# Performance work log

Measured on AMD Instinct MI355X. Metric: run time of the kernel, lower is better.

The kernel has to match this reference:

```python
import jax, jax.numpy as jnp
import numpy as np

V, E, H, M = 256, 512, 512, 128
D = 2 * H  # decoder hidden
B, L_TXT, T_MEL = 32, 256, 800
EPS = 1e-5


def setup_inputs() -> dict:
    key = jax.random.key(0)
    ks = jax.random.split(key, 24)
    s = 0.02
    inp = {
        'x': jax.random.randint(ks[0], (B, L_TXT), 0, V),
        'text_seq_lens': jax.random.randint(ks[1], (B,), 1, L_TXT + 1),
        'y': jax.random.normal(ks[2], (B, T_MEL, M), jnp.float32),
        'mel_spec_lens': jax.random.randint(ks[3], (B,), 1, T_MEL + 1),
        'emb': jax.random.normal(ks[4], (V, E)) * s,
        'conv1_w': jax.random.normal(ks[5], (E, E, 3)) * s,
        'conv1_b': jnp.zeros((E,)),
        'bn1_g': jnp.ones((E,)), 'bn1_b': jnp.zeros((E,)),
        'conv2_w': jax.random.normal(ks[6], (E, E, 3)) * s,
        'conv2_b': jnp.zeros((E,)),
        'bn2_g': jnp.ones((E,)), 'bn2_b': jnp.zeros((E,)),
        'wih_f': jax.random.normal(ks[7], (4 * H, E)) * s,
        'whh_f': jax.random.normal(ks[8], (4 * H, H)) * s,
        'bih_f': jnp.zeros((4 * H,)), 'bhh_f': jnp.zeros((4 * H,)),
        'wih_b': jax.random.normal(ks[9], (4 * H, E)) * s,
        'whh_b': jax.random.normal(ks[10], (4 * H, H)) * s,
        'bih_b': jnp.zeros((4 * H,)), 'bhh_b': jnp.zeros((4 * H,)),
        'dwih': jax.random.normal(ks[11], (4 * D, M)) * s,
        'dwhh': jax.random.normal(ks[12], (4 * D, D)) * s,
        'dbih': jnp.zeros((4 * D,)), 'dbhh': jnp.zeros((4 * D,)),
        'proj_w': jax.random.normal(ks[13], (M, D)) * s,
        'proj_b': jnp.zeros((M,)),
        'gate_w': jax.random.normal(ks[14], (1, D)) * s,
        'gate_b': jnp.zeros((1,)),
    }
    return inp


def _conv_bn_relu(x, w, b, g, beta):
    # x: (B, E, L); training-mode BatchNorm (batch statistics, biased var)
    x = jax.lax.conv_general_dilated(x, w, (1,), [(1, 1)],
                                     dimension_numbers=('NCH', 'OIH', 'NCH')) + b[None, :, None]
    mu = jnp.mean(x, axis=(0, 2), keepdims=True)
    var = jnp.mean((x - mu) ** 2, axis=(0, 2), keepdims=True)
    x = (x - mu) * jax.lax.rsqrt(var + EPS) * g[None, :, None] + beta[None, :, None]
    return jax.nn.relu(x)


def _lstm_last(xseq, lens, wih, whh, bih, bhh):
    # Run LSTM over full padded seq, freezing state past each length.
    # Returns final (h, c) == state at t = len-1 (packed-sequence semantics).
    Bb, T, _ = xseq.shape
    Hh = whh.shape[1]
    pre = jnp.einsum('bte,ge->btg', xseq, wih) + bih + bhh  # (B,T,4H)

    def step(carry, inp):
        h, c = carry
        xt, t = inp
        gates = xt + h @ whh.T
        i, f, g, o = jnp.split(gates, 4, axis=-1)
        c_n = jax.nn.sigmoid(f) * c + jax.nn.sigmoid(i) * jnp.tanh(g)
        h_n = jax.nn.sigmoid(o) * jnp.tanh(c_n)
        valid = (t < lens)[:, None]
        return (jnp.where(valid, h_n, h), jnp.where(valid, c_n, c)), None

    init = (jnp.zeros((Bb, Hh), xseq.dtype), jnp.zeros((Bb, Hh), xseq.dtype))
    (h, c), _ = jax.lax.scan(step, init, (pre.transpose(1, 0, 2), jnp.arange(T)))
    return h, c


def _forward(x, text_seq_lens, y, mel_spec_lens, emb, conv1_w, conv1_b, bn1_g, bn1_b,
             conv2_w, conv2_b, bn2_g, bn2_b, wih_f, whh_f, bih_f, bhh_f,
             wih_b, whh_b, bih_b, bhh_b, dwih, dwhh, dbih, dbhh,
             proj_w, proj_b, gate_w, gate_b):
    xe = emb[x]                       # (B, L, E)
    h = xe.transpose(0, 2, 1)         # (B, E, L)
    h = _conv_bn_relu(h, conv1_w, conv1_b, bn1_g, bn1_b)  # dropout = identity (eval)
    h = _conv_bn_relu(h, conv2_w, conv2_b, bn2_g, bn2_b)
    h = h.transpose(0, 2, 1)          # (B, L, E)

    # bidirectional encoder LSTM final states (packed semantics)
    hf, cf = _lstm_last(h, text_seq_lens, wih_f, whh_f, bih_f, bhh_f)
    # reverse each sequence within its valid length for the backward direction
    t_idx = jnp.arange(h.shape[1])[None, :]
    rev_idx = jnp.clip(text_seq_lens[:, None] - 1 - t_idx, 0, h.shape[1] - 1)
    h_rev = jnp.take_along_axis(h, rev_idx[:, :, None], axis=1)
    hb, cb = _lstm_last(h_rev, text_seq_lens, wih_b, whh_b, bih_b, bhh_b)

    hid = jnp.concatenate([hf, hb], axis=1)  # (B, 2H)
    cel = jnp.concatenate([cf, cb], axis=1)

    Tm = y.shape[1]

    def dec_step(carry, _):
        hd, cd, inp = carry
        gates = inp @ dwih.T + dbih + dbhh + hd @ dwhh.T
        i, f, g, o = jnp.split(gates, 4, axis=-1)
        cd = jax.nn.sigmoid(f) * cd + jax.nn.sigmoid(i) * jnp.tanh(g)
        hd = jax.nn.sigmoid(o) * jnp.tanh(cd)
        mel = hd @ proj_w.T + proj_b          # (B, M)
        gate = hd @ gate_w.T + gate_b         # (B, 1)
        return (hd, cd, mel), (mel, gate[:, 0])

    sos = jnp.zeros((y.shape[0], M), y.dtype)
    _, (mels, gates) = jax.lax.scan(dec_step, (hid, cel, sos), None, length=Tm)
    mel_outputs = mels.transpose(1, 0, 2)     # (B, Tm, M)
    gate_outputs = gates.T                    # (B, Tm)

    mask = jnp.arange(Tm)[None, :] > mel_spec_lens[:, None]  # (B, Tm), strictly >
    masked_mel = jnp.where(mask[:, :, None], 0.0, mel_outputs)
    masked_gate = jnp.where(mask, 1000.0, gate_outputs)
    return masked_mel, masked_gate, mask


def reference(x, text_seq_lens, y, mel_spec_lens, emb, conv1_w, conv1_b, bn1_g, bn1_b,
              conv2_w, conv2_b, bn2_g, bn2_b, wih_f, whh_f, bih_f, bhh_f,
              wih_b, whh_b, bih_b, bhh_b, dwih, dwhh, dbih, dbhh,
              proj_w, proj_b, gate_w, gate_b):
    return _forward(x, text_seq_lens, y, mel_spec_lens, emb, conv1_w, conv1_b,
                    bn1_g, bn1_b, conv2_w, conv2_b, bn2_g, bn2_b,
                    wih_f, whh_f, bih_f, bhh_f, wih_b, whh_b, bih_b, bhh_b,
                    dwih, dwhh, dbih, dbhh, proj_w, proj_b, gate_w, gate_b)
```

## Files before the change

kernel.cpp:

```cpp
#include <hip/hip_runtime.h>


typedef float f4 __attribute__((ext_vector_type(4)));
typedef _Float16 h8 __attribute__((ext_vector_type(8)));
typedef _Float16 half_t;
typedef unsigned long long u64;

#define B_    32
#define LTXT  256
#define TMEL  800
#define EE    512
#define HH    512
#define DD    1024
#define MM    128
#define NROWS 8192
#define GATE_OFF 3276800
#define MASK_OFF 3302400

#define RING_D 801
#define RING_E 257
#define HOP    13

#define WS_MBE        0ull
#define WS_MBD        16384ull
#define WS_HENC       49152ull
#define WS_ZERO_BYTES 81920ull
#define WS_HD         16891904ull
#define WS_BUFX       69386240ull
#define WS_BUFY       77774848ull
#define WS_CONVF      86163456ull
#define WS_WEFF       86163456ull
#define WS_W0         94552064ull
#define WS_WP1        102940672ull
#define WS_WP2        104513536ull
#define WS_WIHP       106086400ull
#define WS_WHHP       110280704ull
#define WS_BSUM       114475008ull
#define WS_BEFF       114491392ull
#define WS_B0         114507776ull
#define WS_MEAN       114524160ull
#define WS_RSTD       114526208ull
#define WS_PROJW      114528256ull
#define WS_PROJG      114790400ull
#define WS_CEL        114823168ull

__device__ __forceinline__ float sigm(float x) { return 1.f / (1.f + __expf(-x)); }
__device__ __forceinline__ float tanh_f(float x) {
    float e = __expf(2.f * x);
    return 1.f - 2.f / (e + 1.f);
}

__device__ __forceinline__ void st_atom64(void* p, u64 v) {
    asm volatile("global_atomic_swap_x2 %0, %1, off" :: "v"(p), "v"(v) : "memory");
}
__device__ __forceinline__ void st_atom32(unsigned* p, unsigned v) {
    asm volatile("global_atomic_swap %0, %1, off" :: "v"(p), "v"(v) : "memory");
}


__global__ void k_embed(const int* __restrict__ x, const float* __restrict__ emb,
                        half_t* __restrict__ out) {
    int row = blockIdx.x;
    int tok = x[row];
    const float* e = emb + (size_t)tok * EE;
    half_t* o = out + (size_t)row * EE;
    for (int c = threadIdx.x; c < EE; c += blockDim.x) o[c] = (half_t)e[c];
}

__global__ void k_packconvw(const float* __restrict__ w, half_t* __restrict__ wp) {
    int idx = blockIdx.x * 256 + threadIdx.x;
    if (idx >= 3 * EE * EE) return;
    int s = idx / (EE * EE);
    int rem = idx - s * EE * EE;
    int eo = rem >> 9, ei = rem & 511;
    wp[idx] = (half_t)w[(size_t)eo * (EE * 3) + ei * 3 + s];
}

__global__ __launch_bounds__(256) void k_conv(const half_t* __restrict__ A,
                                              const half_t* __restrict__ Wp,
                                              const float* __restrict__ bias,
                                              float* __restrict__ out) {
    const int nt = blockIdx.x, et = blockIdx.y;
    const int tid = threadIdx.x;
    const int wv = tid >> 6, l = tid & 63, quad = l >> 4, lo = l & 15;
    const int rowA = nt * 64 + wv * 16 + lo;
    const int eo = et * 16 + lo;
    f4 acc = {0.f, 0.f, 0.f, 0.f};
    for (int s = 0; s < 3; ++s) {
        int lsp = (rowA & 255) + s - 1;
        bool valid = (lsp >= 0) && (lsp < 256);
        int rs = rowA + s - 1;
        rs = rs < 0 ? 0 : (rs > NROWS - 1 ? NROWS - 1 : rs);
        const half_t* ab = A + (size_t)rs * EE;
        const half_t* wb = Wp + ((size_t)s * EE + eo) * EE;
#pragma unroll 4
        for (int ks = 0; ks < 16; ++ks) {
            h8 a = {0, 0, 0, 0, 0, 0, 0, 0};
            if (valid) a = *(const h8*)(ab + ks * 32 + quad * 8);
            h8 b = *(const h8*)(wb + ks * 32 + quad * 8);
            acc = __builtin_amdgcn_mfma_f32_16x16x32_f16(a, b, acc, 0, 0, 0);
        }
    }
    const int orow = nt * 64 + wv * 16 + quad * 4;
    const float bv = bias[eo];
#pragma unroll
    for (int r = 0; r < 4; ++r) out[(size_t)(orow + r) * EE + eo] = acc[r] + bv;
}

__global__ __launch_bounds__(256) void k_bnstats(const float* __restrict__ x,
                                                 float* __restrict__ mean,
                                                 float* __restrict__ rstd) {
    const int c = blockIdx.x;
    float s = 0.f, ss = 0.f;
    for (int n = threadIdx.x; n < NROWS; n += 256) {
        float v = x[(size_t)n * EE + c];
        s += v; ss += v * v;
    }
#pragma unroll
    for (int off = 32; off > 0; off >>= 1) { s += __shfl_down(s, off); ss += __shfl_down(ss, off); }
    __shared__ float as[4], ass[4];
    int wv = threadIdx.x >> 6;
    if ((threadIdx.x & 63) == 0) { as[wv] = s; ass[wv] = ss; }
    __syncthreads();
    if (threadIdx.x == 0) {
        float S = as[0] + as[1] + as[2] + as[3];
        float SS = ass[0] + ass[1] + ass[2] + ass[3];
        float m = S / (float)NROWS;
        float var = SS / (float)NROWS - m * m;
        mean[c] = m;
        rstd[c] = rsqrtf(var + 1e-5f);
    }
}

__global__ void k_bnapply(const float* __restrict__ x, const float* __restrict__ mean,
                          const float* __restrict__ rstd, const float* __restrict__ g,
                          const float* __restrict__ beta, half_t* __restrict__ out) {
    int idx = blockIdx.x * 256 + threadIdx.x;
    if (idx >= NROWS * EE) return;
    int c = idx & (EE - 1);
    float v = (x[idx] - mean[c]) * rstd[c] * g[c] + beta[c];
    out[idx] = (half_t)(v > 0.f ? v : 0.f);
}

__global__ void k_packrec(const float* __restrict__ src, half_t* __restrict__ dst,
                          int Hdim, int kshift, int total) {
    int idx = blockIdx.x * 256 + threadIdx.x;
    if (idx >= total) return;
    int p = idx >> kshift;
    int k = idx & ((1 << kshift) - 1);
    int he = p >> 2, g = p & 3;
    dst[idx] = (half_t)src[((size_t)g * Hdim + he) * (size_t)(1 << kshift) + k];
}

__global__ void k_bsumenc(const float* __restrict__ bf, const float* __restrict__ bhf,
                          const float* __restrict__ bb, const float* __restrict__ bhb,
                          float* __restrict__ bsum) {
    int p = blockIdx.x * 256 + threadIdx.x;
    if (p >= 4096) return;
    int dir = p >> 11, pp = p & 2047;
    int he = pp >> 2, g = pp & 3;
    int row = g * HH + he;
    bsum[p] = dir ? (bb[row] + bhb[row]) : (bf[row] + bhf[row]);
}

__global__ __launch_bounds__(256) void k_weff(const float* __restrict__ dwhh,
                                              const float* __restrict__ dwih,
                                              const float* __restrict__ projw,
                                              half_t* __restrict__ weff,
                                              half_t* __restrict__ w0) {
    int row = blockIdx.x;
    int k = blockIdx.y * 256 + threadIdx.x;
    float v = dwhh[(size_t)row * DD + k];
    float acc = v;
    for (int m = 0; m < MM; ++m) acc += dwih[(size_t)row * MM + m] * projw[(size_t)m * DD + k];
    int p = ((row & (DD - 1)) << 2) | (row >> 10);
    weff[(size_t)p * DD + k] = (half_t)acc;
    w0[(size_t)p * DD + k] = (half_t)v;
}

__global__ void k_bdec(const float* __restrict__ dbih, const float* __restrict__ dbhh,
                       const float* __restrict__ dwih, const float* __restrict__ projb,
                       float* __restrict__ beff, float* __restrict__ b0) {
    int p = blockIdx.x * 256 + threadIdx.x;
    if (p >= 4096) return;
    int he = p >> 2, g = p & 3;
    int row = g * DD + he;
    float bb = dbih[row] + dbhh[row];
    float acc = bb;
    for (int m = 0; m < MM; ++m) acc += dwih[(size_t)row * MM + m] * projb[m];
    b0[p] = bb;
    beff[p] = acc;
}

__global__ void k_cast(const float* __restrict__ src, half_t* __restrict__ dst, int n) {
    int idx = blockIdx.x * 256 + threadIdx.x;
    if (idx < n) dst[idx] = (half_t)src[idx];
}

__global__ void k_projg(const float* __restrict__ gw, half_t* __restrict__ pg) {
    int idx = blockIdx.x * 256 + threadIdx.x;
    if (idx >= 16 * DD) return;
    int row = idx >> 10, k = idx & (DD - 1);
    pg[idx] = (half_t)(row == 0 ? gw[k] : 0.f);
}

__global__ void k_mask(const int* __restrict__ lens, float* __restrict__ out) {
    int idx = blockIdx.x * 256 + threadIdx.x;
    if (idx >= B_ * TMEL) return;
    int b = idx / TMEL, t = idx - b * TMEL;
    out[MASK_OFF + idx] = (t > lens[b]) ? 1.f : 0.f;
}

__global__ __launch_bounds__(512) void k_enc(const half_t* __restrict__ X,
                                             const half_t* __restrict__ wihp,
                                             const half_t* __restrict__ whhp,
                                             const float* __restrict__ bsum,
                                             const int* __restrict__ lens,
                                             half_t* __restrict__ henc,
                                             half_t* __restrict__ hd0,
                                             float* __restrict__ cel,
                                             unsigned* __restrict__ mbE) {
    const int j = blockIdx.x;
    const int dir = j >> 5, sub = j & 31;
    const int tid = threadIdx.x;
    const int wv = tid >> 6, l = tid & 63, quad = l >> 4, lo = l & 15;
    const int rg = wv >> 1, bh = wv & 1;
    const int bfr = bh * 16 + lo;
    const int ue = tid >> 5, ub = tid & 31;

    __shared__ half_t s_hd[32 * 520];
    __shared__ float s_g[32][65];
    __shared__ float s_c[16][32];
    __shared__ float s_h[16][32];
    __shared__ half_t s_hh[16][32];
    __shared__ int s_len[32];

    if (tid < 32) s_len[tid] = lens[tid];
    s_c[ue][ub] = 0.f;
    s_h[ue][ub] = 0.f;

    const int pr = dir * 2048 + sub * 64 + rg * 16 + lo;
    const half_t* wih_b = wihp + (size_t)pr * 512;
    const half_t* whh_b = whhp + (size_t)pr * 512;
    const float bias_n = bsum[pr];

    h8 wihreg[16], whhreg[16];
#pragma unroll
    for (int ks = 0; ks < 16; ++ks) {
        wihreg[ks] = *(const h8*)(wih_b + ks * 32 + quad * 8);
        whhreg[ks] = *(const h8*)(whh_b + ks * 32 + quad * 8);
    }

    int sp = 0, sn = HOP;
    __syncthreads();

    for (int t = 0; t < 256; ++t) {
        if (t > 0) {
            if (tid >= 64 && tid < 96) {
                const unsigned want = (unsigned)t;
                const unsigned* fp = mbE + (size_t)(dir * 32 + sub) * 64 + (tid - 64);
                while (__hip_atomic_load(fp, __ATOMIC_RELAXED, __HIP_MEMORY_SCOPE_AGENT) < want)
                    __builtin_amdgcn_s_sleep(1);
            }
            __syncthreads();
        }

        const half_t* src = henc + (size_t)sp * 32768 + (size_t)dir * 16384;
        h8 tmp0 = *(const h8*)(src + (size_t)(tid + 0 * 512) * 8);
        h8 tmp1 = *(const h8*)(src + (size_t)(tid + 1 * 512) * 8);
        h8 tmp2 = *(const h8*)(src + (size_t)(tid + 2 * 512) * 8);
        h8 tmp3 = *(const h8*)(src + (size_t)(tid + 3 * 512) * 8);

        const int lb = s_len[bfr];
        int tt = (dir == 0) ? t : (lb - 1 - t);
        tt = tt < 0 ? 0 : tt;
        const half_t* xr = X + ((size_t)bfr * 256 + tt) * 512;
        f4 accA = {0.f, 0.f, 0.f, 0.f}, accB = {0.f, 0.f, 0.f, 0.f};
#pragma unroll
        for (int ks = 0; ks < 16; ++ks) {
            h8 a = *(const h8*)(xr + ks * 32 + quad * 8);
            accA = __builtin_amdgcn_mfma_f32_16x16x32_f16(a, wihreg[ks], accA, 0, 0, 0);
        }

        {
            int c0 = tid;
            *(h8*)(s_hd + (size_t)(c0 >> 6) * 520 + (c0 & 63) * 8) = tmp0;
            int c1 = tid + 512;
            *(h8*)(s_hd + (size_t)(c1 >> 6) * 520 + (c1 & 63) * 8) = tmp1;
            int c2 = tid + 1024;
            *(h8*)(s_hd + (size_t)(c2 >> 6) * 520 + (c2 & 63) * 8) = tmp2;
            int c3 = tid + 1536;
            *(h8*)(s_hd + (size_t)(c3 >> 6) * 520 + (c3 & 63) * 8) = tmp3;
        }
        __syncthreads();

#pragma unroll
        for (int ks = 0; ks < 16; ++ks) {
            h8 a = *(const h8*)(s_hd + (size_t)bfr * 520 + ks * 32 + quad * 8);
            accB = __builtin_amdgcn_mfma_f32_16x16x32_f16(a, whhreg[ks], accB, 0, 0, 0);
        }
        const int bm = bh * 16 + quad * 4, cm = rg * 16 + lo;
#pragma unroll
        for (int r = 0; r < 4; ++r) s_g[bm + r][cm] = accA[r] + accB[r] + bias_n;
        __syncthreads();
        {
            float gi = s_g[ub][ue * 4 + 0], gf = s_g[ub][ue * 4 + 1];
            float gg = s_g[ub][ue * 4 + 2], go = s_g[ub][ue * 4 + 3];
            float cn = sigm(gf) * s_c[ue][ub] + sigm(gi) * tanh_f(gg);
            float hn = sigm(go) * tanh_f(cn);
            if (t < s_len[ub]) { s_c[ue][ub] = cn; s_h[ue][ub] = hn; }
            s_hh[ue][ub] = (half_t)s_h[ue][ub];
        }
        __syncthreads();
        if (tid < 64 && t < 255) {
            int b2 = tid >> 1, e8 = (tid & 1) * 8;
            union { half_t h[8]; u64 u[2]; } pk;
#pragma unroll
            for (int i = 0; i < 8; ++i) pk.h[i] = s_hh[e8 + i][b2];
            half_t* dst = henc + (size_t)sn * 32768 + (size_t)dir * 16384
                          + (size_t)b2 * 512 + sub * 16 + e8;
            st_atom64(dst, pk.u[0]);
            st_atom64(dst + 4, pk.u[1]);
            asm volatile("s_waitcnt vmcnt(0)");
            if (tid < 32)
                st_atom32(mbE + ((size_t)(dir * 32 + tid) * 64 + sub), (unsigned)(t + 1));
        }
        if (t < 255) { sp = sn; sn += HOP; if (sn >= RING_E) sn -= RING_E; }
    }
    hd0[(size_t)ub * 1024 + dir * 512 + sub * 16 + ue] = (half_t)s_h[ue][ub];
    cel[(size_t)ub * 1024 + dir * 512 + sub * 16 + ue] = s_c[ue][ub];
}

__global__ __launch_bounds__(512) void k_dec(const half_t* __restrict__ Weff,
                                             const half_t* __restrict__ W0,
                                             const float* __restrict__ beff,
                                             const float* __restrict__ b0,
                                             const half_t* __restrict__ projwb,
                                             const half_t* __restrict__ projg,
                                             const float* __restrict__ projb,
                                             const float* __restrict__ gateb,
                                             const int* __restrict__ mlens,
                                             const float* __restrict__ cel,
                                             half_t* __restrict__ hd,
                                             float* __restrict__ out,
                                             unsigned* __restrict__ mbD) {
    const int j = blockIdx.x;
    const int tid = threadIdx.x;
    const int wv = tid >> 6, l = tid & 63, quad = l >> 4, lo = l & 15;

    __shared__ half_t s_hd[32 * 1032];
    __shared__ float s_g[32][65];
    __shared__ float s_c[16][32];
    __shared__ half_t s_hh[16][32];
    __shared__ int s_len[32];

    if (j < 64) {
        const int rg = wv >> 1, bh = wv & 1;
        const int bfr = bh * 16 + lo;
        const int ue = tid >> 5, ub = tid & 31;

        s_c[ue][ub] = cel[(size_t)ub * 1024 + j * 16 + ue];
        const int pr = j * 64 + rg * 16 + lo;
        const float biasE = beff[pr], bias0 = b0[pr];
        const half_t* wbE = Weff + (size_t)pr * 1024;
        const half_t* wb0 = W0 + (size_t)pr * 1024;

        h8 wreg[32];
#pragma unroll
        for (int ks = 0; ks < 32; ++ks)
            wreg[ks] = *(const h8*)(wbE + ks * 32 + quad * 8);

        int sp = 0, sn = HOP;
        __syncthreads();

        for (int t = 1; t <= TMEL; ++t) {
            if (t > 1) {
                if (tid >= 64 && tid < 128) {
                    const unsigned want = (unsigned)(t - 1);
                    const unsigned* fp = mbD + (size_t)j * 64 + (tid - 64);
                    while (__hip_atomic_load(fp, __ATOMIC_RELAXED, __HIP_MEMORY_SCOPE_AGENT) < want)
                        __builtin_amdgcn_s_sleep(1);
                }
                __syncthreads();
            }

            const half_t* src = hd + (size_t)sp * 32768;
            {
                h8 tp[8];
#pragma unroll
                for (int i = 0; i < 8; ++i)
                    tp[i] = *(const h8*)(src + (size_t)(tid + i * 512) * 8);
#pragma unroll
                for (int i = 0; i < 8; ++i) {
                    int c = tid + i * 512;
                    *(h8*)(s_hd + (size_t)(c >> 7) * 1032 + (c & 127) * 8) = tp[i];
                }
            }
            __syncthreads();

            const half_t* ar = s_hd + (size_t)bfr * 1032 + quad * 8;
            f4 acc = {0.f, 0.f, 0.f, 0.f}, acc2 = {0.f, 0.f, 0.f, 0.f};
            if (t == 1) {
#pragma unroll 8
                for (int ks = 0; ks < 32; ks += 2) {
                    h8 a0 = *(const h8*)(ar + ks * 32);
                    h8 a1 = *(const h8*)(ar + ks * 32 + 32);
                    acc = __builtin_amdgcn_mfma_f32_16x16x32_f16(a0, *(const h8*)(wb0 + ks * 32 + quad * 8), acc, 0, 0, 0);
                    acc2 = __builtin_amdgcn_mfma_f32_16x16x32_f16(a1, *(const h8*)(wb0 + ks * 32 + 32 + quad * 8), acc2, 0, 0, 0);
                }
            } else {
#pragma unroll
                for (int ks = 0; ks < 32; ks += 2) {
                    h8 a0 = *(const h8*)(ar + ks * 32);
                    h8 a1 = *(const h8*)(ar + ks * 32 + 32);
                    acc = __builtin_amdgcn_mfma_f32_16x16x32_f16(a0, wreg[ks], acc, 0, 0, 0);
                    acc2 = __builtin_amdgcn_mfma_f32_16x16x32_f16(a1, wreg[ks + 1], acc2, 0, 0, 0);
                }
            }
            const float bn = (t == 1) ? bias0 : biasE;
            const int bm = bh * 16 + quad * 4, cm = rg * 16 + lo;
#pragma unroll
            for (int r = 0; r < 4; ++r) s_g[bm + r][cm] = acc[r] + acc2[r] + bn;
            __syncthreads();
            {
                float gi = s_g[ub][ue * 4 + 0], gf = s_g[ub][ue * 4 + 1];
                float gg = s_g[ub][ue * 4 + 2], go = s_g[ub][ue * 4 + 3];
                float cn = sigm(gf) * s_c[ue][ub] + sigm(gi) * tanh_f(gg);
                s_c[ue][ub] = cn;
                s_hh[ue][ub] = (half_t)(sigm(go) * tanh_f(cn));
            }
            __syncthreads();
            if (tid < 64) {
                int b2 = tid >> 1, e8 = (tid & 1) * 8;
                union { half_t h[8]; u64 u[2]; } pk;
#pragma unroll
                for (int i = 0; i < 8; ++i) pk.h[i] = s_hh[e8 + i][b2];
                half_t* dst = hd + (size_t)sn * 32768 + (size_t)b2 * 1024 + j * 16 + e8;
                st_atom64(dst, pk.u[0]);
                st_atom64(dst + 4, pk.u[1]);
                asm volatile("s_waitcnt vmcnt(0)");
                st_atom32(mbD + ((size_t)tid * 64 + j), (unsigned)t);
                if (tid < 9)
                    st_atom32(mbD + ((size_t)(64 + tid) * 64 + j), (unsigned)t);
            }
            sp = sn; sn += HOP; if (sn >= RING_D) sn -= RING_D;
        }
    } else {
        const int pj = j - 64;
        const bool meld = (pj < 8);
        const bool duty = (wv < 2);
        const int bh2 = wv & 1;
        const half_t* pw = meld ? (projwb + (size_t)(pj * 16 + lo) * 1024)
                                : (projg + (size_t)lo * 1024);
        const float biasP = meld ? projb[pj * 16 + lo] : gateb[0];

        h8 pwreg[32];
        if (duty) {
#pragma unroll
            for (int ks = 0; ks < 32; ++ks)
                pwreg[ks] = *(const h8*)(pw + ks * 32 + quad * 8);
        }
        if (tid < 32) s_len[tid] = mlens[tid];

        int spP = HOP;
        __syncthreads();

        for (int t = 1; t <= TMEL; ++t) {
            if (tid < 64) {
                const unsigned want = (unsigned)t;
                const unsigned* fp = mbD + (size_t)(64 + pj) * 64 + tid;
                while (__hip_atomic_load(fp, __ATOMIC_RELAXED, __HIP_MEMORY_SCOPE_AGENT) < want)
                    __builtin_amdgcn_s_sleep(1);
            }
            __syncthreads();

            const half_t* src = hd + (size_t)spP * 32768;
            {
                h8 tp[8];
#pragma unroll
                for (int i = 0; i < 8; ++i)
                    tp[i] = *(const h8*)(src + (size_t)(tid + i * 512) * 8);
#pragma unroll
                for (int i = 0; i < 8; ++i) {
                    int c = tid + i * 512;
                    *(h8*)(s_hd + (size_t)(c >> 7) * 1032 + (c & 127) * 8) = tp[i];
                }
            }
            __syncthreads();

            if (duty) {
                const half_t* ar = s_hd + (size_t)(bh2 * 16 + lo) * 1032 + quad * 8;
                f4 accm = {0.f, 0.f, 0.f, 0.f}, accm2 = {0.f, 0.f, 0.f, 0.f};
#pragma unroll
                for (int ks = 0; ks < 32; ks += 2) {
                    h8 a0 = *(const h8*)(ar + ks * 32);
                    h8 a1 = *(const h8*)(ar + ks * 32 + 32);
                    accm = __builtin_amdgcn_mfma_f32_16x16x32_f16(a0, pwreg[ks], accm, 0, 0, 0);
                    accm2 = __builtin_amdgcn_mfma_f32_16x16x32_f16(a1, pwreg[ks + 1], accm2, 0, 0, 0);
                }
                accm[0] += accm2[0]; accm[1] += accm2[1];
                accm[2] += accm2[2]; accm[3] += accm2[3];
                const int pos = t - 1;
                if (meld) {
#pragma unroll
                    for (int r = 0; r < 4; ++r) {
                        int b = bh2 * 16 + quad * 4 + r;
                        float v = accm[r] + biasP;
                        if (pos > s_len[b]) v = 0.f;
                        __builtin_nontemporal_store(v,
                            &out[(size_t)b * (TMEL * MM) + (size_t)pos * MM + pj * 16 + lo]);
                    }
                } else if (lo == 0) {
#pragma unroll
                    for (int r = 0; r < 4; ++r) {
                        int b = bh2 * 16 + quad * 4 + r;
                        float v = accm[r] + biasP;
                        if (pos > s_len[b]) v = 1000.f;
                        __builtin_nontemporal_store(v, &out[GATE_OFF + (size_t)b * TMEL + pos]);
                    }
                }
            }
            __syncthreads();
            spP += HOP; if (spP >= RING_D) spP -= RING_D;
        }
    }
}


extern "C" void kernel_launch(void* const* d_in, const int* in_sizes, int n_in,
                              void* d_out, int out_size, void* d_ws, size_t ws_size,
                              hipStream_t stream) {
    const int* x = (const int*)d_in[0];
    const int* tlens = (const int*)d_in[1];
    const int* mlens = (const int*)d_in[3];
    const float* emb = (const float*)d_in[4];
    const float* c1w = (const float*)d_in[5];
    const float* c1b = (const float*)d_in[6];
    const float* bn1g = (const float*)d_in[7];
    const float* bn1b = (const float*)d_in[8];
    const float* c2w = (const float*)d_in[9];
    const float* c2b = (const float*)d_in[10];
    const float* bn2g = (const float*)d_in[11];
    const float* bn2b = (const float*)d_in[12];
    const float* wihf = (const float*)d_in[13];
    const float* whhf = (const float*)d_in[14];
    const float* bihf = (const float*)d_in[15];
    const float* bhhf = (const float*)d_in[16];
    const float* wihb = (const float*)d_in[17];
    const float* whhb = (const float*)d_in[18];
    const float* bihb = (const float*)d_in[19];
    const float* bhhb = (const float*)d_in[20];
    const float* dwih = (const float*)d_in[21];
    const float* dwhh = (const float*)d_in[22];
    const float* dbih = (const float*)d_in[23];
    const float* dbhh = (const float*)d_in[24];
    const float* projw = (const float*)d_in[25];
    const float* projb = (const float*)d_in[26];
    const float* gatew = (const float*)d_in[27];
    const float* gateb = (const float*)d_in[28];
    float* out = (float*)d_out;
    char* ws = (char*)d_ws;

    unsigned* mbE = (unsigned*)(ws + WS_MBE);
    unsigned* mbD = (unsigned*)(ws + WS_MBD);
    half_t* henc = (half_t*)(ws + WS_HENC);
    half_t* hd = (half_t*)(ws + WS_HD);
    half_t* bufX = (half_t*)(ws + WS_BUFX);
    half_t* bufY = (half_t*)(ws + WS_BUFY);
    float* convf = (float*)(ws + WS_CONVF);
    half_t* weff = (half_t*)(ws + WS_WEFF);
    half_t* w0 = (half_t*)(ws + WS_W0);
    half_t* wp1 = (half_t*)(ws + WS_WP1);
    half_t* wp2 = (half_t*)(ws + WS_WP2);
    float* meanb = (float*)(ws + WS_MEAN);
    float* rstdb = (float*)(ws + WS_RSTD);
    half_t* wihp = (half_t*)(ws + WS_WIHP);
    half_t* whhp = (half_t*)(ws + WS_WHHP);
    float* bsum = (float*)(ws + WS_BSUM);
    float* beff = (float*)(ws + WS_BEFF);
    float* b0 = (float*)(ws + WS_B0);
    half_t* projwb = (half_t*)(ws + WS_PROJW);
    half_t* projg = (half_t*)(ws + WS_PROJG);
    float* cel = (float*)(ws + WS_CEL);

    hipMemsetAsync(d_ws, 0, (size_t)WS_ZERO_BYTES, stream);

    k_embed<<<NROWS, 256, 0, stream>>>(x, emb, bufX);
    k_packconvw<<<(3 * EE * EE + 255) / 256, 256, 0, stream>>>(c1w, wp1);
    k_conv<<<dim3(128, 32), 256, 0, stream>>>(bufX, wp1, c1b, convf);
    k_bnstats<<<EE, 256, 0, stream>>>(convf, meanb, rstdb);
    k_bnapply<<<(NROWS * EE) / 256, 256, 0, stream>>>(convf, meanb, rstdb, bn1g, bn1b, bufY);
    k_packconvw<<<(3 * EE * EE + 255) / 256, 256, 0, stream>>>(c2w, wp2);
    k_conv<<<dim3(128, 32), 256, 0, stream>>>(bufY, wp2, c2b, convf);
    k_bnstats<<<EE, 256, 0, stream>>>(convf, meanb, rstdb);
    k_bnapply<<<(NROWS * EE) / 256, 256, 0, stream>>>(convf, meanb, rstdb, bn2g, bn2b, bufX);

    const int encTot = 2048 * 512;
    k_packrec<<<(encTot + 255) / 256, 256, 0, stream>>>(wihf, wihp, HH, 9, encTot);
    k_packrec<<<(encTot + 255) / 256, 256, 0, stream>>>(wihb, wihp + encTot, HH, 9, encTot);
    k_packrec<<<(encTot + 255) / 256, 256, 0, stream>>>(whhf, whhp, HH, 9, encTot);
    k_packrec<<<(encTot + 255) / 256, 256, 0, stream>>>(whhb, whhp + encTot, HH, 9, encTot);
    k_bsumenc<<<16, 256, 0, stream>>>(bihf, bhhf, bihb, bhhb, bsum);

    k_enc<<<64, 512, 0, stream>>>(bufX, wihp, whhp, bsum, tlens, henc, hd, cel, mbE);

    k_weff<<<dim3(4096, 4), 256, 0, stream>>>(dwhh, dwih, projw, weff, w0);
    k_bdec<<<16, 256, 0, stream>>>(dbih, dbhh, dwih, projb, beff, b0);
    k_cast<<<(MM * DD + 255) / 256, 256, 0, stream>>>(projw, projwb, MM * DD);
    k_projg<<<(16 * DD + 255) / 256, 256, 0, stream>>>(gatew, projg);

    k_dec<<<73, 512, 0, stream>>>(weff, w0, beff, b0, projwb, projg, projb, gateb,
                                  mlens, cel, hd, out, mbD);

    k_mask<<<(B_ * TMEL + 255) / 256, 256, 0, stream>>>(mlens, out);

    (void)in_sizes; (void)n_in; (void)out_size; (void)ws_size;
}
```

Measured before the change: 4.901 ms.

## Split decoder recurrence into two independent batch groups with separate rings and mailboxes

The persistent decoder kernel now splits the batch of 32 into two independent groups of 16. Each group has its own hidden-state ring, its own mailbox flags and 32 recurrent blocks, with each block covering 128 gate rows instead of 64. Each group's blocks only wait on the 32 blocks of their own group, so there are fewer flags to poll and less hidden state to copy into shared memory per step. The projection and gate blocks are reorganised into one pair per group. The trade-off is that each block now loads weights for twice as many rows, and the encoder's final hidden-state write and the zeroed workspace size change to match the new layout.

Measured after the change: 4.482 ms. 8.6% less time.

```diff
diff --git a/kernel.cpp b/kernel.cpp
--- a/kernel.cpp
+++ b/kernel.cpp
@@ -24,7 +24,7 @@
 #define WS_MBE        0ull
 #define WS_MBD        16384ull
 #define WS_HENC       49152ull
-#define WS_ZERO_BYTES 81920ull
+#define WS_ZERO_BYTES 114688ull
 #define WS_HD         16891904ull
 #define WS_BUFX       69386240ull
 #define WS_BUFY       77774848ull
@@ -217,7 +217,7 @@
                                              const float* __restrict__ bsum,
                                              const int* __restrict__ lens,
                                              half_t* __restrict__ henc,
-                                             half_t* __restrict__ hd0,
+                                             half_t* __restrict__ hd,
                                              float* __restrict__ cel,
                                              unsigned* __restrict__ mbE) {
     const int j = blockIdx.x;
@@ -327,7 +327,11 @@
         }
         if (t < 255) { sp = sn; sn += HOP; if (sn >= RING_E) sn -= RING_E; }
     }
-    hd0[(size_t)ub * 1024 + dir * 512 + sub * 16 + ue] = (half_t)s_h[ue][ub];
+    {
+        int g2 = ub >> 4, b = ub & 15;
+        hd[(size_t)g2 * ((size_t)RING_D * 16384) + (size_t)b * 1024
+           + dir * 512 + sub * 16 + ue] = (half_t)s_h[ue][ub];
+    }
     cel[(size_t)ub * 1024 + dir * 512 + sub * 16 + ue] = s_c[ue][ub];
 }
 
@@ -348,19 +352,21 @@
     const int tid = threadIdx.x;
     const int wv = tid >> 6, l = tid & 63, quad = l >> 4, lo = l & 15;
 
-    __shared__ half_t s_hd[32 * 1032];
-    __shared__ float s_g[32][65];
-    __shared__ float s_c[16][32];
-    __shared__ half_t s_hh[16][32];
+    __shared__ half_t s_hd[16 * 1032];
+    __shared__ float s_g[16][129];
+    __shared__ float s_c[32][16];
+    __shared__ half_t s_hh[32][16];
     __shared__ int s_len[32];
 
     if (j < 64) {
-        const int rg = wv >> 1, bh = wv & 1;
-        const int bfr = bh * 16 + lo;
-        const int ue = tid >> 5, ub = tid & 31;
-
-        s_c[ue][ub] = cel[(size_t)ub * 1024 + j * 16 + ue];
-        const int pr = j * 64 + rg * 16 + lo;
+        const int g = j >> 5, jj = j & 31;
+        half_t* hdG = hd + (size_t)g * ((size_t)RING_D * 16384);
+        unsigned* mbG = mbD + (size_t)g * 34 * 64;
+        const int ue = tid >> 4;
+        const int ub = tid & 15;
+
+        s_c[ue][ub] = cel[(size_t)(g * 16 + ub) * 1024 + jj * 32 + ue];
+        const int pr = jj * 128 + wv * 16 + lo;
         const float biasE = beff[pr], bias0 = b0[pr];
         const half_t* wbE = Weff + (size_t)pr * 1024;
         const half_t* wb0 = W0 + (size_t)pr * 1024;
@@ -375,30 +381,30 @@
 
         for (int t = 1; t <= TMEL; ++t) {
             if (t > 1) {
-                if (tid >= 64 && tid < 128) {
+                if (tid >= 64 && tid < 96) {
                     const unsigned want = (unsigned)(t - 1);
-                    const unsigned* fp = mbD + (size_t)j * 64 + (tid - 64);
+                    const unsigned* fp = mbG + (size_t)jj * 64 + (tid - 64);
                     while (__hip_atomic_load(fp, __ATOMIC_RELAXED, __HIP_MEMORY_SCOPE_AGENT) < want)
                         __builtin_amdgcn_s_sleep(1);
                 }
                 __syncthreads();
             }
 
-            const half_t* src = hd + (size_t)sp * 32768;
             {
-                h8 tp[8];
-#pragma unroll
-                for (int i = 0; i < 8; ++i)
+                const half_t* src = hdG + (size_t)sp * 16384;
+                h8 tp[4];
+#pragma unroll
+                for (int i = 0; i < 4; ++i)
                     tp[i] = *(const h8*)(src + (size_t)(tid + i * 512) * 8);
 #pragma unroll
-                for (int i = 0; i < 8; ++i) {
+                for (int i = 0; i < 4; ++i) {
                     int c = tid + i * 512;
                     *(h8*)(s_hd + (size_t)(c >> 7) * 1032 + (c & 127) * 8) = tp[i];
                 }
             }
             __syncthreads();
 
-            const half_t* ar = s_hd + (size_t)bfr * 1032 + quad * 8;
+            const half_t* ar = s_hd + (size_t)lo * 1032 + quad * 8;
             f4 acc = {0.f, 0.f, 0.f, 0.f}, acc2 = {0.f, 0.f, 0.f, 0.f};
             if (t == 1) {
 #pragma unroll 8
@@ -418,9 +424,8 @@
                 }
             }
             const float bn = (t == 1) ? bias0 : biasE;
-            const int bm = bh * 16 + quad * 4, cm = rg * 16 + lo;
-#pragma unroll
-            for (int r = 0; r < 4; ++r) s_g[bm + r][cm] = acc[r] + acc2[r] + bn;
+#pragma unroll
+            for (int r = 0; r < 4; ++r) s_g[quad * 4 + r][wv * 16 + lo] = acc[r] + acc2[r] + bn;
             __syncthreads();
             {
                 float gi = s_g[ub][ue * 4 + 0], gf = s_g[ub][ue * 4 + 1];
@@ -431,28 +436,30 @@
             }
             __syncthreads();
             if (tid < 64) {
-                int b2 = tid >> 1, e8 = (tid & 1) * 8;
+                int b2 = tid >> 2, e8 = (tid & 3) * 8;
                 union { half_t h[8]; u64 u[2]; } pk;
 #pragma unroll
                 for (int i = 0; i < 8; ++i) pk.h[i] = s_hh[e8 + i][b2];
-                half_t* dst = hd + (size_t)sn * 32768 + (size_t)b2 * 1024 + j * 16 + e8;
+                half_t* dst = hdG + (size_t)sn * 16384 + (size_t)b2 * 1024 + jj * 32 + e8;
                 st_atom64(dst, pk.u[0]);
                 st_atom64(dst + 4, pk.u[1]);
                 asm volatile("s_waitcnt vmcnt(0)");
-                st_atom32(mbD + ((size_t)tid * 64 + j), (unsigned)t);
-                if (tid < 9)
-                    st_atom32(mbD + ((size_t)(64 + tid) * 64 + j), (unsigned)t);
+                if (tid < 34)
+                    st_atom32(mbG + ((size_t)tid * 64 + jj), (unsigned)t);
             }
             sp = sn; sn += HOP; if (sn >= RING_D) sn -= RING_D;
         }
     } else {
-        const int pj = j - 64;
-        const bool meld = (pj < 8);
-        const bool duty = (wv < 2);
-        const int bh2 = wv & 1;
-        const half_t* pw = meld ? (projwb + (size_t)(pj * 16 + lo) * 1024)
+        const int p = j - 64;
+        const int g = p >> 1;
+        const bool meld = ((p & 1) == 0);
+        half_t* hdG = hd + (size_t)g * ((size_t)RING_D * 16384);
+        unsigned* mbG = mbD + (size_t)g * 34 * 64;
+        const int cons = meld ? 32 : 33;
+        const bool duty = meld || (wv == 0);
+        const half_t* pw = meld ? (projwb + (size_t)(wv * 16 + lo) * 1024)
                                 : (projg + (size_t)lo * 1024);
-        const float biasP = meld ? projb[pj * 16 + lo] : gateb[0];
+        const float biasP = meld ? projb[wv * 16 + lo] : gateb[0];
 
         h8 pwreg[32];
         if (duty) {
@@ -466,22 +473,22 @@
         __syncthreads();
 
         for (int t = 1; t <= TMEL; ++t) {
-            if (tid < 64) {
+            if (tid < 32) {
                 const unsigned want = (unsigned)t;
-                const unsigned* fp = mbD + (size_t)(64 + pj) * 64 + tid;
+                const unsigned* fp = mbG + (size_t)cons * 64 + tid;
                 while (__hip_atomic_load(fp, __ATOMIC_RELAXED, __HIP_MEMORY_SCOPE_AGENT) < want)
                     __builtin_amdgcn_s_sleep(1);
             }
             __syncthreads();
 
-            const half_t* src = hd + (size_t)spP * 32768;
             {
-                h8 tp[8];
-#pragma unroll
-                for (int i = 0; i < 8; ++i)
+                const half_t* src = hdG + (size_t)spP * 16384;
+                h8 tp[4];
+#pragma unroll
+                for (int i = 0; i < 4; ++i)
                     tp[i] = *(const h8*)(src + (size_t)(tid + i * 512) * 8);
 #pragma unroll
-                for (int i = 0; i < 8; ++i) {
+                for (int i = 0; i < 4; ++i) {
                     int c = tid + i * 512;
                     *(h8*)(s_hd + (size_t)(c >> 7) * 1032 + (c & 127) * 8) = tp[i];
                 }
@@ -489,7 +496,7 @@
             __syncthreads();
 
             if (duty) {
-                const half_t* ar = s_hd + (size_t)(bh2 * 16 + lo) * 1032 + quad * 8;
+                const half_t* ar = s_hd + (size_t)lo * 1032 + quad * 8;
                 f4 accm = {0.f, 0.f, 0.f, 0.f}, accm2 = {0.f, 0.f, 0.f, 0.f};
 #pragma unroll
                 for (int ks = 0; ks < 32; ks += 2) {
@@ -504,16 +511,16 @@
                 if (meld) {
 #pragma unroll
                     for (int r = 0; r < 4; ++r) {
-                        int b = bh2 * 16 + quad * 4 + r;
+                        int b = g * 16 + quad * 4 + r;
                         float v = accm[r] + biasP;
                         if (pos > s_len[b]) v = 0.f;
                         __builtin_nontemporal_store(v,
-                            &out[(size_t)b * (TMEL * MM) + (size_t)pos * MM + pj * 16 + lo]);
+                            &out[(size_t)b * (TMEL * MM) + (size_t)pos * MM + wv * 16 + lo]);
                     }
                 } else if (lo == 0) {
 #pragma unroll
                     for (int r = 0; r < 4; ++r) {
-                        int b = bh2 * 16 + quad * 4 + r;
+                        int b = g * 16 + quad * 4 + r;
                         float v = accm[r] + biasP;
                         if (pos > s_len[b]) v = 1000.f;
                         __builtin_nontemporal_store(v, &out[GATE_OFF + (size_t)b * TMEL + pos]);
@@ -609,7 +616,7 @@
     k_cast<<<(MM * DD + 255) / 256, 256, 0, stream>>>(projw, projwb, MM * DD);
     k_projg<<<(16 * DD + 255) / 256, 256, 0, stream>>>(gatew, projg);
 
-    k_dec<<<73, 512, 0, stream>>>(weff, w0, beff, b0, projwb, projg, projb, gateb,
+    k_dec<<<68, 512, 0, stream>>>(weff, w0, beff, b0, projwb, projg, projb, gateb,
                                   mlens, cel, hd, out, mbD);
 
     k_mask<<<(B_ * TMEL + 255) / 256, 256, 0, stream>>>(mlens, out);
```
